# Kernel tuning notes

Hardware: AMD Instinct MI355X
Metric: run time of the kernel (lower is better)

Reference implementation:

```python
import jax, jax.numpy as jnp
import numpy as np

B, T, H = 4, 4096, 1024
E = 8                      # num_experts
K = 2                      # experts_per_token
F = 4096 // E * 2          # expert_ffn_dim = 1024
LB_COEFF = 0.01


def setup_inputs() -> dict:
    key = jax.random.key(0)
    ks = jax.random.split(key, 5)
    s = 0.02
    return {
        "x": jax.random.normal(ks[0], (B, T, H), dtype=jnp.float32),
        "router_w": jax.random.normal(ks[1], (E, H), dtype=jnp.float32) * s,   # Linear weight [out,in]
        "gate_w": jax.random.normal(ks[2], (E, F, H), dtype=jnp.float32) * s,
        "up_w": jax.random.normal(ks[3], (E, F, H), dtype=jnp.float32) * s,
        "down_w": jax.random.normal(ks[4], (E, H, F), dtype=jnp.float32) * s,
    }


def reference(x, router_w, gate_w, up_w, down_w):
    b, t, h = x.shape
    xf = x.reshape(-1, h)                              # [N,H]
    n = xf.shape[0]
    logits = xf @ router_w.T                           # [N,E]
    probs = jax.nn.softmax(logits, axis=-1)
    top_v, top_i = jax.lax.top_k(probs, K)             # [N,K]
    top_v = top_v / jnp.sum(top_v, axis=-1, keepdims=True)
    # dense gate matrix: gates[n,e] = normalized prob if expert e in top-k of token n else 0
    gates = jnp.zeros_like(probs).at[jnp.arange(n)[:, None], top_i].set(top_v)  # [N,E]
    out = jnp.zeros_like(xf)
    for e in range(E):  # small fixed expert loop; SwiGLU FFN per expert, gated combine
        hid = jax.nn.silu(xf @ gate_w[e].T) * (xf @ up_w[e].T)   # [N,F]
        out = out + gates[:, e:e + 1] * (hid @ down_w[e].T)      # weighted scatter-add
    out = out.reshape(b, t, h)
    usage = probs.mean(axis=0)                          # [E]
    lb_loss = LB_COEFF * (E * jnp.sum(usage * usage))
    return out, lb_loss
```

## Files before the change

kernel.cpp:

```cpp
#include <hip/hip_runtime.h>
#include <math.h>

#define N_TOK 16384
#define HD    1024
#define FD    1024
#define NE    8
#define NA    (N_TOK * 2)
#define MBLK  128
#define MAX_MB 264

typedef __attribute__((ext_vector_type(8))) short bf16x8;
typedef __attribute__((ext_vector_type(4))) short bf16x4;
typedef __attribute__((ext_vector_type(4))) float f32x4;

#define WS_USAGE  0u
#define WS_COUNTS 64u
#define WS_OFFS   128u
#define WS_CURSOR 192u
#define WS_TBLN   256u
#define WS_BLKE   320u
#define WS_BLKM   (WS_BLKE + 1088u)
#define WS_TOKE   8192u
#define WS_TOKG   (WS_TOKE + NA * 4u)
#define WS_TOKP   (WS_TOKG + NA * 4u)
#define WS_ATOK   (WS_TOKP + NA * 4u)
#define WS_AGATE  (WS_ATOK + NA * 4u)
#define WS_XB     (1u << 20)
#define WS_GWB    (WS_XB  + 33554432u)
#define WS_UWB    (WS_GWB + 16777216u)
#define WS_DWB    (WS_UWB + 16777216u)
#define WS_HID    (WS_DWB + 16777216u)
#define WS_Y      WS_XB

__device__ __forceinline__ short f2b(float f) {
    union { float f; unsigned u; } c;
    c.f = f;
    unsigned u = (c.u + 0x7fffu + ((c.u >> 16) & 1u)) >> 16;
    return (short)u;
}
__device__ __forceinline__ float b2f(short s) {
    union { unsigned u; float f; } c;
    c.u = ((unsigned)(unsigned short)s) << 16;
    return c.f;
}

__device__ __forceinline__ void gl_lds16(const short* g, short* l) {
    __builtin_amdgcn_global_load_lds(
        (const __attribute__((address_space(1))) unsigned int*)g,
        (__attribute__((address_space(3))) unsigned int*)l,
        16, 0, 0);
}

__global__ void init_kernel(int* ws) {
    if (threadIdx.x < 64) ws[threadIdx.x] = 0;
}

__global__ __launch_bounds__(256) void cvt3_kernel(
    const float* __restrict__ gw, const float* __restrict__ uw, const float* __restrict__ dw,
    short* __restrict__ gwb, short* __restrict__ uwb, short* __restrict__ dwb) {
    const float* in  = (blockIdx.y == 0) ? gw  : (blockIdx.y == 1) ? uw  : dw;
    short*       out = (blockIdx.y == 0) ? gwb : (blockIdx.y == 1) ? uwb : dwb;
    const int i = blockIdx.x * 256 + threadIdx.x;
    const float4 a = ((const float4*)in)[2 * i];
    const float4 b = ((const float4*)in)[2 * i + 1];
    bf16x8 o;
    o[0] = f2b(a.x); o[1] = f2b(a.y); o[2] = f2b(a.z); o[3] = f2b(a.w);
    o[4] = f2b(b.x); o[5] = f2b(b.y); o[6] = f2b(b.z); o[7] = f2b(b.w);
    ((bf16x8*)out)[i] = o;
}

__global__ __launch_bounds__(256) void router_kernel(
    const float* __restrict__ x, const float* __restrict__ rw,
    float* __restrict__ usage, int* __restrict__ counts,
    int* __restrict__ tok_e, float* __restrict__ tok_g, short* __restrict__ xb)
{
    __shared__ float rws[NE * HD];
    __shared__ float usage_s[NE];
    __shared__ int counts_s[NE];
    const int tid = threadIdx.x;
    if (tid < NE) { usage_s[tid] = 0.f; counts_s[tid] = 0; }
    for (int c = tid; c < NE * HD / 4; c += 256)
        ((float4*)rws)[c] = ((const float4*)rw)[c];
    __syncthreads();

    const int wave = tid >> 6, lane = tid & 63;
    const int t = blockIdx.x * 4 + wave;
    float acc[NE];
#pragma unroll
    for (int e = 0; e < NE; ++e) acc[e] = 0.f;
    const float* xrow = x + (size_t)t * HD;
    short* xbrow = xb + (size_t)t * HD;
#pragma unroll
    for (int j = 0; j < 4; ++j) {
        const int h0 = (j * 64 + lane) * 4;
        const float4 xv = *(const float4*)(xrow + h0);
        bf16x4 xc;
        xc[0] = f2b(xv.x); xc[1] = f2b(xv.y); xc[2] = f2b(xv.z); xc[3] = f2b(xv.w);
        *(bf16x4*)(xbrow + h0) = xc;
#pragma unroll
        for (int e = 0; e < NE; ++e) {
            const float4 wv = *(const float4*)&rws[e * HD + h0];
            acc[e] += xv.x * wv.x + xv.y * wv.y + xv.z * wv.z + xv.w * wv.w;
        }
    }
#pragma unroll
    for (int e = 0; e < NE; ++e)
#pragma unroll
        for (int off = 32; off > 0; off >>= 1)
            acc[e] += __shfl_xor(acc[e], off, 64);

    if (lane == 0) {
        float mx = acc[0];
        for (int e = 1; e < NE; ++e) mx = fmaxf(mx, acc[e]);
        float p[NE], Z = 0.f;
        for (int e = 0; e < NE; ++e) { p[e] = expf(acc[e] - mx); Z += p[e]; }
        const float invZ = 1.f / Z;
        for (int e = 0; e < NE; ++e) { p[e] *= invZ; atomicAdd(&usage_s[e], p[e]); }
        int i0 = 0;
        for (int e = 1; e < NE; ++e) if (acc[e] > acc[i0]) i0 = e;
        int i1 = (i0 == 0) ? 1 : 0;
        for (int e = 0; e < NE; ++e) if (e != i0 && acc[e] > acc[i1]) i1 = e;
        const float gs = 1.f / (p[i0] + p[i1]);
        tok_e[2 * t] = i0;  tok_e[2 * t + 1] = i1;
        tok_g[2 * t] = p[i0] * gs;  tok_g[2 * t + 1] = p[i1] * gs;
        atomicAdd(&counts_s[i0], 1); atomicAdd(&counts_s[i1], 1);
    }
    __syncthreads();
    if (tid < NE) {
        atomicAdd(&usage[tid], usage_s[tid]);
        atomicAdd(&counts[tid], counts_s[tid]);
    }
}

__global__ void offsets_lb_kernel(const float* __restrict__ usage,
                                  const int* __restrict__ counts,
                                  int* __restrict__ offs, float* __restrict__ lb_out,
                                  int* __restrict__ tbl_n, int* __restrict__ blk_e,
                                  int* __restrict__ blk_m)
{
    if (threadIdx.x == 0) {
        int acc = 0, nb = 0;
        for (int e = 0; e < NE; ++e) {
            offs[e] = acc;
            const int c = counts[e];
            acc += c;
            for (int mb = 0; mb < c; mb += MBLK) { blk_e[nb] = e; blk_m[nb] = mb; ++nb; }
        }
        offs[NE] = acc;
        tbl_n[0] = nb;
        float s = 0.f;
        for (int e = 0; e < NE; ++e) {
            const float u = usage[e] * (1.f / (float)N_TOK);
            s += u * u;
        }
        lb_out[0] = 0.01f * 8.f * s;
    }
}

__global__ __launch_bounds__(256) void scatter_kernel(
    const int* __restrict__ tok_e, const float* __restrict__ tok_g,
    const int* __restrict__ offs, int* __restrict__ cursor,
    int* __restrict__ asg_tok, float* __restrict__ asg_g,
    int* __restrict__ tok_pos)
{
    __shared__ int cnt_s[NE];
    __shared__ int base_s[NE];
    const int tid = threadIdx.x;
    if (tid < NE) cnt_s[tid] = 0;
    __syncthreads();

    const int idx = blockIdx.x * 256 + tid;
    const int e = tok_e[idx];
    const int local = atomicAdd(&cnt_s[e], 1);
    __syncthreads();

    if (tid < NE) base_s[tid] = atomicAdd(&cursor[tid], cnt_s[tid]);
    __syncthreads();

    const int pos = offs[e] + base_s[e] + local;
    asg_tok[pos] = idx >> 1;
    asg_g[pos] = tok_g[idx];
    tok_pos[idx] = pos;
}


__global__ __launch_bounds__(256, 4) void gemm1_kernel(
    const short* __restrict__ xb, const short* __restrict__ gate_b,
    const short* __restrict__ up_b, const int* __restrict__ counts,
    const int* __restrict__ offs, const int* __restrict__ asg_tok,
    const int* __restrict__ tbl_n, const int* __restrict__ blk_e,
    const int* __restrict__ blk_m, short* __restrict__ hid)
{
    __shared__ short As[128 * 64];
    __shared__ short Bg[64 * 64];
    __shared__ short Bu[64 * 64];

    const int wg  = blockIdx.x;
    const int swz = (wg & 7) * (16 * MAX_MB / 8) + (wg >> 3);
    const int m_id = swz >> 4;
    const int n_base = (swz & 15) * 64;
    if (m_id >= tbl_n[0]) return;
    const int e = blk_e[m_id];
    const int m_base = blk_m[m_id];
    const int n_e = counts[e];
    const int off_e = offs[e];

    const int tid = threadIdx.x;
    const int wave = tid >> 6, lane = tid & 63;
    const int lr = lane >> 3, lg = lane & 7;
    const int sg = lg ^ lr;

    const short* a_src[4];
#pragma unroll
    for (int j = 0; j < 4; ++j) {
        const int r = wave * 32 + j * 8 + lr;
        const int gm = m_base + r;
        const int tok = asg_tok[off_e + (gm < n_e ? gm : 0)];
        a_src[j] = xb + (size_t)tok * HD + sg * 8;
    }
    const short* gwp = gate_b + (size_t)e * FD * HD;
    const short* uwp = up_b + (size_t)e * FD * HD;
    const short* bg_src[2]; const short* bu_src[2];
#pragma unroll
    for (int j = 0; j < 2; ++j) {
        const int r = wave * 16 + j * 8 + lr;
        bg_src[j] = gwp + (size_t)(n_base + r) * HD + sg * 8;
        bu_src[j] = uwp + (size_t)(n_base + r) * HD + sg * 8;
    }

    const int wm = (wave >> 1) * 64;
    const int wn = (wave & 1) * 32;
    const int quad = lane >> 4, l16 = lane & 15;

    f32x4 accG[4][2], accU[4][2];
#pragma unroll
    for (int mi = 0; mi < 4; ++mi)
#pragma unroll
        for (int ni = 0; ni < 2; ++ni) { accG[mi][ni] = (f32x4){0,0,0,0}; accU[mi][ni] = (f32x4){0,0,0,0}; }

    for (int t = 0; t < 16; ++t) {
        const int k0 = t * 64;
#pragma unroll
        for (int j = 0; j < 4; ++j)
            gl_lds16(a_src[j] + k0, &As[(wave * 32 + j * 8) * 64]);
#pragma unroll
        for (int j = 0; j < 2; ++j) {
            gl_lds16(bg_src[j] + k0, &Bg[(wave * 16 + j * 8) * 64]);
            gl_lds16(bu_src[j] + k0, &Bu[(wave * 16 + j * 8) * 64]);
        }
        __syncthreads();
#pragma unroll
        for (int kk8 = 0; kk8 < 8; kk8 += 4) {
            bf16x8 a[4];
#pragma unroll
            for (int mi = 0; mi < 4; ++mi) {
                const int row = wm + mi * 16 + l16;
                const int pg = (kk8 + quad) ^ (row & 7);
                a[mi] = *(const bf16x8*)&As[row * 64 + pg * 8];
            }
#pragma unroll
            for (int ni = 0; ni < 2; ++ni) {
                const int row = wn + ni * 16 + l16;
                const int pg = (kk8 + quad) ^ (row & 7);
                bf16x8 bg = *(const bf16x8*)&Bg[row * 64 + pg * 8];
                bf16x8 bu = *(const bf16x8*)&Bu[row * 64 + pg * 8];
#pragma unroll
                for (int mi = 0; mi < 4; ++mi) {
                    accG[mi][ni] = __builtin_amdgcn_mfma_f32_16x16x32_bf16(a[mi], bg, accG[mi][ni], 0, 0, 0);
                    accU[mi][ni] = __builtin_amdgcn_mfma_f32_16x16x32_bf16(a[mi], bu, accU[mi][ni], 0, 0, 0);
                }
            }
        }
        __syncthreads();
    }

#pragma unroll
    for (int mi = 0; mi < 4; ++mi) {
#pragma unroll
        for (int r = 0; r < 4; ++r) {
            const int gm = m_base + wm + mi * 16 + quad * 4 + r;
            if (gm < n_e) {
#pragma unroll
                for (int ni = 0; ni < 2; ++ni) {
                    const int f = n_base + wn + ni * 16 + l16;
                    const float gv = accG[mi][ni][r];
                    const float uv = accU[mi][ni][r];
                    hid[(size_t)(off_e + gm) * FD + f] = f2b((gv / (1.f + expf(-gv))) * uv);
                }
            }
        }
    }
}

__global__ __launch_bounds__(256, 4) void gemm2_kernel(
    const short* __restrict__ hid, const short* __restrict__ down_b,
    const int* __restrict__ counts, const int* __restrict__ offs,
    const float* __restrict__ asg_g, const int* __restrict__ tbl_n,
    const int* __restrict__ blk_e, const int* __restrict__ blk_m,
    short* __restrict__ Y)
{
    __shared__ short As[128 * 64];
    __shared__ short Bs[128 * 64];

    const int wg  = blockIdx.x;
    const int swz = (wg & 7) * (8 * MAX_MB / 8) + (wg >> 3);
    const int m_id = swz >> 3;
    const int n_base = (swz & 7) * 128;
    if (m_id >= tbl_n[0]) return;
    const int e = blk_e[m_id];
    const int m_base = blk_m[m_id];
    const int n_e = counts[e];
    const int off_e = offs[e];

    const int tid = threadIdx.x;
    const int wave = tid >> 6, lane = tid & 63;
    const int lr = lane >> 3, lg = lane & 7;
    const int sg = lg ^ lr;

    const short* a_src[4]; const short* b_src[4];
    const short* bwp = down_b + (size_t)e * HD * FD;
#pragma unroll
    for (int j = 0; j < 4; ++j) {
        const int r = wave * 32 + j * 8 + lr;
        const int gm = m_base + r;
        const size_t srow = (size_t)(off_e + (gm < n_e ? gm : 0));
        a_src[j] = hid + srow * FD + sg * 8;
        b_src[j] = bwp + (size_t)(n_base + r) * FD + sg * 8;
    }

    const int wm = (wave >> 1) * 64;
    const int wn = (wave & 1) * 64;
    const int quad = lane >> 4, l16 = lane & 15;

    f32x4 acc[4][4];
#pragma unroll
    for (int mi = 0; mi < 4; ++mi)
#pragma unroll
        for (int ni = 0; ni < 4; ++ni) acc[mi][ni] = (f32x4){0,0,0,0};

    for (int t = 0; t < 16; ++t) {
        const int k0 = t * 64;
#pragma unroll
        for (int j = 0; j < 4; ++j) {
            gl_lds16(a_src[j] + k0, &As[(wave * 32 + j * 8) * 64]);
            gl_lds16(b_src[j] + k0, &Bs[(wave * 32 + j * 8) * 64]);
        }
        __syncthreads();
#pragma unroll
        for (int kk8 = 0; kk8 < 8; kk8 += 4) {
            bf16x8 a[4], b[4];
#pragma unroll
            for (int mi = 0; mi < 4; ++mi) {
                const int row = wm + mi * 16 + l16;
                const int pg = (kk8 + quad) ^ (row & 7);
                a[mi] = *(const bf16x8*)&As[row * 64 + pg * 8];
            }
#pragma unroll
            for (int ni = 0; ni < 4; ++ni) {
                const int row = wn + ni * 16 + l16;
                const int pg = (kk8 + quad) ^ (row & 7);
                b[ni] = *(const bf16x8*)&Bs[row * 64 + pg * 8];
            }
#pragma unroll
            for (int mi = 0; mi < 4; ++mi)
#pragma unroll
                for (int ni = 0; ni < 4; ++ni)
                    acc[mi][ni] = __builtin_amdgcn_mfma_f32_16x16x32_bf16(a[mi], b[ni], acc[mi][ni], 0, 0, 0);
        }
        __syncthreads();
    }

#pragma unroll
    for (int mi = 0; mi < 4; ++mi) {
#pragma unroll
        for (int r = 0; r < 4; ++r) {
            const int gm = m_base + wm + mi * 16 + quad * 4 + r;
            if (gm < n_e) {
                const int pos = off_e + gm;
                const float gate = asg_g[pos];
                short* yrow = Y + (size_t)pos * HD;
#pragma unroll
                for (int ni = 0; ni < 4; ++ni) {
                    const int n = n_base + wn + ni * 16 + l16;
                    yrow[n] = f2b(acc[mi][ni][r] * gate);
                }
            }
        }
    }
}

__global__ __launch_bounds__(256) void combine_kernel(
    const short* __restrict__ Y, const int* __restrict__ tok_pos, float* __restrict__ out)
{
    const int g = blockIdx.x * 256 + threadIdx.x;
    const int t  = g >> 7;
    const int w8 = (g & 127) * 8;
    const int p0 = tok_pos[2 * t], p1 = tok_pos[2 * t + 1];
    const bf16x8 y0 = *(const bf16x8*)(Y + (size_t)p0 * HD + w8);
    const bf16x8 y1 = *(const bf16x8*)(Y + (size_t)p1 * HD + w8);
    float4 o0, o1;
    o0.x = b2f(y0[0]) + b2f(y1[0]); o0.y = b2f(y0[1]) + b2f(y1[1]);
    o0.z = b2f(y0[2]) + b2f(y1[2]); o0.w = b2f(y0[3]) + b2f(y1[3]);
    o1.x = b2f(y0[4]) + b2f(y1[4]); o1.y = b2f(y0[5]) + b2f(y1[5]);
    o1.z = b2f(y0[6]) + b2f(y1[6]); o1.w = b2f(y0[7]) + b2f(y1[7]);
    float* orow = out + (size_t)t * HD + w8;
    *(float4*)orow = o0;
    *(float4*)(orow + 4) = o1;
}

extern "C" void kernel_launch(void* const* d_in, const int* in_sizes, int n_in,
                              void* d_out, int out_size, void* d_ws, size_t ws_size,
                              hipStream_t stream)
{
    const float* x  = (const float*)d_in[0];
    const float* rw = (const float*)d_in[1];
    const float* gw = (const float*)d_in[2];
    const float* uw = (const float*)d_in[3];
    const float* dw = (const float*)d_in[4];
    float* out = (float*)d_out;

    char* ws = (char*)d_ws;
    float* usage = (float*)(ws + WS_USAGE);
    int* counts  = (int*)(ws + WS_COUNTS);
    int* offs    = (int*)(ws + WS_OFFS);
    int* cursor  = (int*)(ws + WS_CURSOR);
    int* tbl_n   = (int*)(ws + WS_TBLN);
    int* blk_e   = (int*)(ws + WS_BLKE);
    int* blk_m   = (int*)(ws + WS_BLKM);
    int* tok_e   = (int*)(ws + WS_TOKE);
    float* tok_g = (float*)(ws + WS_TOKG);
    int* tok_pos = (int*)(ws + WS_TOKP);
    int* asg_tok = (int*)(ws + WS_ATOK);
    float* asg_g = (float*)(ws + WS_AGATE);
    short* xb    = (short*)(ws + WS_XB);
    short* gwb   = (short*)(ws + WS_GWB);
    short* uwb   = (short*)(ws + WS_UWB);
    short* dwb   = (short*)(ws + WS_DWB);
    short* hid   = (short*)(ws + WS_HID);
    short* Y     = (short*)(ws + WS_Y);

    init_kernel<<<1, 64, 0, stream>>>((int*)ws);
    cvt3_kernel<<<dim3((NE * FD * HD / 8) / 256, 3), 256, 0, stream>>>(gw, uw, dw, gwb, uwb, dwb);
    router_kernel<<<N_TOK / 4, 256, 0, stream>>>(x, rw, usage, counts, tok_e, tok_g, xb);
    offsets_lb_kernel<<<1, 64, 0, stream>>>(usage, counts, offs, out + 16777216,
                                            tbl_n, blk_e, blk_m);
    scatter_kernel<<<NA / 256, 256, 0, stream>>>(tok_e, tok_g, offs, cursor,
                                                 asg_tok, asg_g, tok_pos);
    gemm1_kernel<<<16 * MAX_MB, 256, 0, stream>>>(
        xb, gwb, uwb, counts, offs, asg_tok, tbl_n, blk_e, blk_m, hid);
    gemm2_kernel<<<8 * MAX_MB, 256, 0, stream>>>(
        hid, dwb, counts, offs, asg_g, tbl_n, blk_e, blk_m, Y);
    combine_kernel<<<(N_TOK * HD / 8) / 256, 256, 0, stream>>>(Y, tok_pos, out);
}
```

Baseline: 482.8 us.

## Double the M tile of both expert GEMMs to 256 rows

Raises the per-workgroup M block from 128 to 256 rows in both grouped GEMMs, so each wave computes 128 rows and the expert weight tiles are loaded half as often per token. The A-fragment loads are moved inside the mi loop to keep register pressure down, and the staging row mapping is interleaved across waves. Occupancy hint drops from 4 to 2 workgroups per CU, and padding waste per expert grows with the larger block.

```diff
diff --git a/kernel.cpp b/kernel.cpp
--- a/kernel.cpp
+++ b/kernel.cpp
@@ -6,8 +6,8 @@
 #define FD    1024
 #define NE    8
 #define NA    (N_TOK * 2)
-#define MBLK  128
-#define MAX_MB 264
+#define MBLK  256
+#define MAX_MB 136
 
 typedef __attribute__((ext_vector_type(8))) short bf16x8;
 typedef __attribute__((ext_vector_type(4))) short bf16x4;
@@ -184,14 +184,14 @@
 }
 
 
-__global__ __launch_bounds__(256, 4) void gemm1_kernel(
+__global__ __launch_bounds__(256, 2) void gemm1_kernel(
     const short* __restrict__ xb, const short* __restrict__ gate_b,
     const short* __restrict__ up_b, const int* __restrict__ counts,
     const int* __restrict__ offs, const int* __restrict__ asg_tok,
     const int* __restrict__ tbl_n, const int* __restrict__ blk_e,
     const int* __restrict__ blk_m, short* __restrict__ hid)
 {
-    __shared__ short As[128 * 64];
+    __shared__ short As[256 * 64];
     __shared__ short Bg[64 * 64];
     __shared__ short Bu[64 * 64];
 
@@ -210,10 +210,10 @@
     const int lr = lane >> 3, lg = lane & 7;
     const int sg = lg ^ lr;
 
-    const short* a_src[4];
-#pragma unroll
-    for (int j = 0; j < 4; ++j) {
-        const int r = wave * 32 + j * 8 + lr;
+    const short* a_src[8];
+#pragma unroll
+    for (int j = 0; j < 8; ++j) {
+        const int r = j * 32 + wave * 8 + lr;
         const int gm = m_base + r;
         const int tok = asg_tok[off_e + (gm < n_e ? gm : 0)];
         a_src[j] = xb + (size_t)tok * HD + sg * 8;
@@ -223,51 +223,51 @@
     const short* bg_src[2]; const short* bu_src[2];
 #pragma unroll
     for (int j = 0; j < 2; ++j) {
-        const int r = wave * 16 + j * 8 + lr;
+        const int r = j * 32 + wave * 8 + lr;
         bg_src[j] = gwp + (size_t)(n_base + r) * HD + sg * 8;
         bu_src[j] = uwp + (size_t)(n_base + r) * HD + sg * 8;
     }
 
-    const int wm = (wave >> 1) * 64;
+    const int wm = (wave >> 1) * 128;
     const int wn = (wave & 1) * 32;
     const int quad = lane >> 4, l16 = lane & 15;
 
-    f32x4 accG[4][2], accU[4][2];
-#pragma unroll
-    for (int mi = 0; mi < 4; ++mi)
+    f32x4 accG[8][2], accU[8][2];
+#pragma unroll
+    for (int mi = 0; mi < 8; ++mi)
 #pragma unroll
         for (int ni = 0; ni < 2; ++ni) { accG[mi][ni] = (f32x4){0,0,0,0}; accU[mi][ni] = (f32x4){0,0,0,0}; }
 
     for (int t = 0; t < 16; ++t) {
         const int k0 = t * 64;
 #pragma unroll
-        for (int j = 0; j < 4; ++j)
-            gl_lds16(a_src[j] + k0, &As[(wave * 32 + j * 8) * 64]);
+        for (int j = 0; j < 8; ++j)
+            gl_lds16(a_src[j] + k0, &As[(j * 32 + wave * 8) * 64]);
 #pragma unroll
         for (int j = 0; j < 2; ++j) {
-            gl_lds16(bg_src[j] + k0, &Bg[(wave * 16 + j * 8) * 64]);
-            gl_lds16(bu_src[j] + k0, &Bu[(wave * 16 + j * 8) * 64]);
+            gl_lds16(bg_src[j] + k0, &Bg[(j * 32 + wave * 8) * 64]);
+            gl_lds16(bu_src[j] + k0, &Bu[(j * 32 + wave * 8) * 64]);
         }
         __syncthreads();
 #pragma unroll
         for (int kk8 = 0; kk8 < 8; kk8 += 4) {
-            bf16x8 a[4];
-#pragma unroll
-            for (int mi = 0; mi < 4; ++mi) {
-                const int row = wm + mi * 16 + l16;
-                const int pg = (kk8 + quad) ^ (row & 7);
-                a[mi] = *(const bf16x8*)&As[row * 64 + pg * 8];
-            }
+            bf16x8 bg[2], bu[2];
 #pragma unroll
             for (int ni = 0; ni < 2; ++ni) {
                 const int row = wn + ni * 16 + l16;
                 const int pg = (kk8 + quad) ^ (row & 7);
-                bf16x8 bg = *(const bf16x8*)&Bg[row * 64 + pg * 8];
-                bf16x8 bu = *(const bf16x8*)&Bu[row * 64 + pg * 8];
-#pragma unroll
-                for (int mi = 0; mi < 4; ++mi) {
-                    accG[mi][ni] = __builtin_amdgcn_mfma_f32_16x16x32_bf16(a[mi], bg, accG[mi][ni], 0, 0, 0);
-                    accU[mi][ni] = __builtin_amdgcn_mfma_f32_16x16x32_bf16(a[mi], bu, accU[mi][ni], 0, 0, 0);
+                bg[ni] = *(const bf16x8*)&Bg[row * 64 + pg * 8];
+                bu[ni] = *(const bf16x8*)&Bu[row * 64 + pg * 8];
+            }
+#pragma unroll
+            for (int mi = 0; mi < 8; ++mi) {
+                const int row = wm + mi * 16 + l16;
+                const int pg = (kk8 + quad) ^ (row & 7);
+                const bf16x8 a = *(const bf16x8*)&As[row * 64 + pg * 8];
+#pragma unroll
+                for (int ni = 0; ni < 2; ++ni) {
+                    accG[mi][ni] = __builtin_amdgcn_mfma_f32_16x16x32_bf16(a, bg[ni], accG[mi][ni], 0, 0, 0);
+                    accU[mi][ni] = __builtin_amdgcn_mfma_f32_16x16x32_bf16(a, bu[ni], accU[mi][ni], 0, 0, 0);
                 }
             }
         }
@@ -275,7 +275,7 @@
     }
 
 #pragma unroll
-    for (int mi = 0; mi < 4; ++mi) {
+    for (int mi = 0; mi < 8; ++mi) {
 #pragma unroll
         for (int r = 0; r < 4; ++r) {
             const int gm = m_base + wm + mi * 16 + quad * 4 + r;
@@ -292,14 +292,14 @@
     }
 }
 
-__global__ __launch_bounds__(256, 4) void gemm2_kernel(
+__global__ __launch_bounds__(256, 2) void gemm2_kernel(
     const short* __restrict__ hid, const short* __restrict__ down_b,
     const int* __restrict__ counts, const int* __restrict__ offs,
     const float* __restrict__ asg_g, const int* __restrict__ tbl_n,
     const int* __restrict__ blk_e, const int* __restrict__ blk_m,
     short* __restrict__ Y)
 {
-    __shared__ short As[128 * 64];
+    __shared__ short As[256 * 64];
     __shared__ short Bs[128 * 64];
 
     const int wg  = blockIdx.x;
@@ -317,44 +317,43 @@
     const int lr = lane >> 3, lg = lane & 7;
     const int sg = lg ^ lr;
 
-    const short* a_src[4]; const short* b_src[4];
+    const short* a_src[8]; const short* b_src[4];
     const short* bwp = down_b + (size_t)e * HD * FD;
 #pragma unroll
-    for (int j = 0; j < 4; ++j) {
-        const int r = wave * 32 + j * 8 + lr;
+    for (int j = 0; j < 8; ++j) {
+        const int r = j * 32 + wave * 8 + lr;
         const int gm = m_base + r;
         const size_t srow = (size_t)(off_e + (gm < n_e ? gm : 0));
         a_src[j] = hid + srow * FD + sg * 8;
+    }
+#pragma unroll
+    for (int j = 0; j < 4; ++j) {
+        const int r = j * 32 + wave * 8 + lr;
         b_src[j] = bwp + (size_t)(n_base + r) * FD + sg * 8;
     }
 
-    const int wm = (wave >> 1) * 64;
+    const int wm = (wave >> 1) * 128;
     const int wn = (wave & 1) * 64;
     const int quad = lane >> 4, l16 = lane & 15;
 
-    f32x4 acc[4][4];
-#pragma unroll
-    for (int mi = 0; mi < 4; ++mi)
+    f32x4 acc[8][4];
+#pragma unroll
+    for (int mi = 0; mi < 8; ++mi)
 #pragma unroll
         for (int ni = 0; ni < 4; ++ni) acc[mi][ni] = (f32x4){0,0,0,0};
 
     for (int t = 0; t < 16; ++t) {
         const int k0 = t * 64;
 #pragma unroll
-        for (int j = 0; j < 4; ++j) {
-            gl_lds16(a_src[j] + k0, &As[(wave * 32 + j * 8) * 64]);
-            gl_lds16(b_src[j] + k0, &Bs[(wave * 32 + j * 8) * 64]);
-        }
+        for (int j = 0; j < 8; ++j)
+            gl_lds16(a_src[j] + k0, &As[(j * 32 + wave * 8) * 64]);
+#pragma unroll
+        for (int j = 0; j < 4; ++j)
+            gl_lds16(b_src[j] + k0, &Bs[(j * 32 + wave * 8) * 64]);
         __syncthreads();
 #pragma unroll
         for (int kk8 = 0; kk8 < 8; kk8 += 4) {
-            bf16x8 a[4], b[4];
-#pragma unroll
-            for (int mi = 0; mi < 4; ++mi) {
-                const int row = wm + mi * 16 + l16;
-                const int pg = (kk8 + quad) ^ (row & 7);
-                a[mi] = *(const bf16x8*)&As[row * 64 + pg * 8];
-            }
+            bf16x8 b[4];
 #pragma unroll
             for (int ni = 0; ni < 4; ++ni) {
                 const int row = wn + ni * 16 + l16;
@@ -362,16 +361,20 @@
                 b[ni] = *(const bf16x8*)&Bs[row * 64 + pg * 8];
             }
 #pragma unroll
-            for (int mi = 0; mi < 4; ++mi)
+            for (int mi = 0; mi < 8; ++mi) {
+                const int row = wm + mi * 16 + l16;
+                const int pg = (kk8 + quad) ^ (row & 7);
+                const bf16x8 a = *(const bf16x8*)&As[row * 64 + pg * 8];
 #pragma unroll
                 for (int ni = 0; ni < 4; ++ni)
-                    acc[mi][ni] = __builtin_amdgcn_mfma_f32_16x16x32_bf16(a[mi], b[ni], acc[mi][ni], 0, 0, 0);
+                    acc[mi][ni] = __builtin_amdgcn_mfma_f32_16x16x32_bf16(a, b[ni], acc[mi][ni], 0, 0, 0);
+            }
         }
         __syncthreads();
     }
 
 #pragma unroll
-    for (int mi = 0; mi < 4; ++mi) {
+    for (int mi = 0; mi < 8; ++mi) {
 #pragma unroll
         for (int r = 0; r < 4; ++r) {
             const int gm = m_base + wm + mi * 16 + quad * 4 + r;
```

Measured after the change: 520.7 us. 1.08x slower.
